# Optimization experiments

Hardware: AMD Instinct MI355X
Metric: run time of the kernel (lower is better)

Reference implementation:

```python
import jax, jax.numpy as jnp
import numpy as np

DIM, H, MAX_K, RADIUS, KNN_K, ALPHA, LN_EPS = 128, 4, 32, 0.3, 8, 2, 1e-5
DH = DIM // H
SCALE = DH ** -0.5


def _layernorm(x, w, b):
    mu = jnp.mean(x, axis=-1, keepdims=True)
    var = jnp.mean((x - mu) ** 2, axis=-1, keepdims=True)
    return (x - mu) * jax.lax.rsqrt(var + LN_EPS) * w + b


def setup_inputs() -> dict:
    key = jax.random.key(0)
    ks = jax.random.split(key, 12)
    N, M = 50000, 2500
    init = lambda k, shape: (jax.random.normal(k, shape, jnp.float32) * 0.02)
    return {
        "xyz": jax.random.normal(ks[0], (N, 3), jnp.float32),
        "feats": jax.random.normal(ks[1], (N, DIM), jnp.float32),
        "Wq": init(ks[2], (DIM, DIM)),
        "Wk": init(ks[3], (DIM, DIM)),
        "Wv": init(ks[4], (DIM, DIM)),
        "Wo": init(ks[5], (DIM, DIM)),
        "bo": jnp.zeros((DIM,), jnp.float32),
        "n1w": jnp.ones((DIM,), jnp.float32),
        "n1b": jnp.zeros((DIM,), jnp.float32),
        "n2w": jnp.ones((DIM,), jnp.float32),
        "n2b": jnp.zeros((DIM,), jnp.float32),
        "W1": init(ks[6], (DIM, 4 * DIM)),
        "b1": jnp.zeros((4 * DIM,), jnp.float32),
        "W2": init(ks[7], (4 * DIM, DIM)),
        "b2": jnp.zeros((DIM,), jnp.float32),
        "Wp": init(ks[8], (DIM, DIM)),
        "bp": jnp.zeros((DIM,), jnp.float32),
        "idx_center": jax.random.randint(ks[9], (M,), 0, N),
    }


def reference(xyz, feats, Wq, Wk, Wv, Wo, bo, n1w, n1b, n2w, n2b, W1, b1, W2, b2, Wp, bp, idx_center):
    M = idx_center.shape[0]
    center_xyz = xyz[idx_center]          # (M,3)
    center_feat = feats[idx_center]       # (M,C)

    # euclidean distance matrix (M,N) via |a|^2+|b|^2-2ab, safe sqrt (0-grad at 0 like torch.cdist)
    d2 = (jnp.sum(center_xyz ** 2, -1)[:, None] + jnp.sum(xyz ** 2, -1)[None, :]
          - 2.0 * center_xyz @ xyz.T)
    d2 = jnp.maximum(d2, 0.0)
    pos = d2 > 0
    dist = jnp.where(pos, jnp.sqrt(jnp.where(pos, d2, 1.0)), 0.0)  # (M,N)

    # ball query: mask + top-max_k smallest distances
    nbr_mask = dist < RADIUS
    nbr_mask = nbr_mask.at[jnp.arange(M), idx_center].set(True)
    dist_masked = jnp.where(nbr_mask, dist, jnp.inf)
    neg_d, nbr_idx = jax.lax.top_k(-dist_masked, MAX_K)   # (M,K)
    nbr_dist = -neg_d
    mask_valid = jnp.isfinite(nbr_dist)                    # (M,K)

    # gather neighbor feats, zero where invalid
    nbr_feats = jnp.where(mask_valid[..., None], feats[nbr_idx], 0.0)  # (M,K,C)

    # masked local attention per center (tiny heads)
    q = (center_feat @ Wq).reshape(M, H, DH)                       # (M,H,D)
    k = (nbr_feats @ Wk).reshape(M, MAX_K, H, DH).transpose(0, 2, 1, 3)  # (M,H,K,D)
    v = (nbr_feats @ Wv).reshape(M, MAX_K, H, DH).transpose(0, 2, 1, 3)
    attn = jnp.einsum('mhd,mhkd->mhk', q * SCALE, k)
    attn = jnp.where(mask_valid[:, None, :], attn, -1e9)
    attn = jax.nn.softmax(attn, axis=-1)
    out = jnp.einsum('mhk,mhkd->mhd', attn, v)
    # faithful to torch: transpose(1,2) before flatten -> (M, D, H) layout
    out = jnp.swapaxes(out, 1, 2).reshape(M, DIM)
    upd = out @ Wo + bo

    cf = center_feat + _layernorm(upd, n1w, n1b)
    ffn = jax.nn.relu(cf @ W1 + b1) @ W2 + b2
    cf = cf + _layernorm(ffn, n2w, n2b)

    # KNN inverse-distance-weighted upsample back to all N points
    neg_v, knn_idx = jax.lax.top_k(-dist.T, KNN_K)   # (N,k)
    knn_dist = -neg_v
    w = 1.0 / (knn_dist + 1e-6) ** ALPHA
    w = w / jnp.sum(w, axis=-1, keepdims=True)
    out_feats = jnp.einsum('nk,nkc->nc', w, cf[knn_idx])  # (N,C)
    out_feats = out_feats + jax.nn.relu(out_feats @ Wp + bp)
    return feats + out_feats
```

## Files before the change

### kernel.cpp

```cpp
#include <hip/hip_runtime.h>
#include <hip/hip_bf16.h>
#include <stdint.h>

#define DIM    128
#define KMAX   32
#define LN_EPS 1e-5f
#define ATT_SCALE 0.17677669529663687f
#define CANDB  1024
#define WTOT   214400
#define PB     32
#define CH     64
#define GSTR   68

typedef unsigned long long u64;
static __device__ __forceinline__ float bf2f(__hip_bfloat16 x) { return __bfloat162float(x); }

static __device__ __forceinline__ float norm32(float x, float y, float z) {
    return __fadd_rn(__fadd_rn(__fmul_rn(x, x), __fmul_rn(y, y)), __fmul_rn(z, z));
}
static __device__ __forceinline__ float d2_32(float cx, float cy, float cz, float cw,
                                              float px, float py, float pz, float pw) {
    float dot = __fmaf_rn(cz, pz, __fmaf_rn(cy, py, __fmul_rn(cx, px)));
    return __fsub_rn(__fadd_rn(cw, pw), __fmul_rn(2.0f, dot));
}
static __device__ __forceinline__ float d2_to_dist(float d2) {
    d2 = fmaxf(d2, 0.0f);
    return (d2 > 0.0f) ? __fsqrt_rn(d2) : 0.0f;
}
static __device__ __forceinline__ float dist32(float cx, float cy, float cz, float cw,
                                               float px, float py, float pz, float pw) {
    return d2_to_dist(d2_32(cx, cy, cz, cw, px, py, pz, pw));
}

static __device__ __forceinline__ float ldf(const void* p, int f32, size_t i) {
    return f32 ? ((const float*)p)[i] : bf2f(((const __hip_bfloat16*)p)[i]);
}
static __device__ __forceinline__ int ldidx(const void* p, int i64, int m) {
    return i64 ? ((const int*)p)[2 * m] : ((const int*)p)[m];
}

struct Ptrs { const void* p[18]; int sz[18]; };

__global__ void probe_dtypes(Ptrs P, int* __restrict__ fl) {
    int j = threadIdx.x;
    if (j >= 18) return;
    const void* x = P.p[j];
    int sz = P.sz[j];
    int flag = 0;
    if (j == 17) {
        const int* ip = (const int*)x;
        int odd_zero = 1, even_nz = 0;
        for (int k = 0; k < 8 && 2 * k + 1 < sz * 2; ++k) {
            if (ip[2 * k + 1] != 0) odd_zero = 0;
            if (ip[2 * k] != 0) even_nz = 1;
        }
        flag = (odd_zero && even_nz) ? 1 : 0;
    } else {
        const __hip_bfloat16* hp = (const __hip_bfloat16*)x;
        int n = sz < 256 ? sz : 256;
        for (int i = 0; i < n; ++i) {
            float w = bf2f(hp[i]);
            if (w != w || fabsf(w) > 1000.0f) { flag = 1; break; }
        }
        if ((j == 7 || j == 9) && bf2f(hp[0]) == 0.0f) flag = 1;
    }
    fl[j] = flag;
}

__global__ __launch_bounds__(256) void conv_prep(Ptrs P, const int* __restrict__ fl,
                                                 float* __restrict__ Wf,
                                                 float4* __restrict__ pnt4,
                                                 float4* __restrict__ cent4,
                                                 int N, int M, int convB) {
    int b = blockIdx.x;
    if (b < convB) {
        int i = b * 256 + threadIdx.x;
        if (i >= WTOT) return;
        int j, off;
        if      (i < 16384)  { j = 2;  off = i; }
        else if (i < 32768)  { j = 3;  off = i - 16384; }
        else if (i < 49152)  { j = 4;  off = i - 32768; }
        else if (i < 65536)  { j = 5;  off = i - 49152; }
        else if (i < 131072) { j = 11; off = i - 65536; }
        else if (i < 196608) { j = 13; off = i - 131072; }
        else if (i < 212992) { j = 15; off = i - 196608; }
        else if (i < 213120) { j = 6;  off = i - 212992; }
        else if (i < 213248) { j = 7;  off = i - 213120; }
        else if (i < 213376) { j = 8;  off = i - 213248; }
        else if (i < 213504) { j = 9;  off = i - 213376; }
        else if (i < 213632) { j = 10; off = i - 213504; }
        else if (i < 214144) { j = 12; off = i - 213632; }
        else if (i < 214272) { j = 14; off = i - 214144; }
        else                 { j = 16; off = i - 214272; }
        Wf[i] = ldf(P.p[j], fl[j], off);
    } else {
        int i = (b - convB) * 256 + threadIdx.x;
        int f0 = fl[0];
        if (i < N) {
            float x = ldf(P.p[0], f0, 3 * i + 0);
            float y = ldf(P.p[0], f0, 3 * i + 1);
            float z = ldf(P.p[0], f0, 3 * i + 2);
            pnt4[i] = make_float4(x, y, z, norm32(x, y, z));
        }
        if (i < M) {
            int c = ldidx(P.p[17], fl[17], i);
            c = (c >= 0 && c < N) ? c : 0;
            float x = ldf(P.p[0], f0, 3 * c + 0);
            float y = ldf(P.p[0], f0, 3 * c + 1);
            float z = ldf(P.p[0], f0, 3 * c + 2);
            cent4[i] = make_float4(x, y, z, norm32(x, y, z));
        }
    }
}

__global__ __launch_bounds__(256, 8) void ball_scan(
    const float4* __restrict__ pnt4,
    const float4* __restrict__ cent4,
    int N, int M, int* __restrict__ nbr_g) {

    __shared__ u64 key[2][CANDB];
    __shared__ int s_cnt[2], s_ni[2][KMAX];

    int tid = threadIdx.x;
    int m0 = blockIdx.x * 2, m1 = m0 + 1;
    bool has1 = (m1 < M);
    float4 c0 = cent4[m0];
    float4 c1 = has1 ? cent4[m1] : make_float4(1e30f, 1e30f, 1e30f, 1e30f);

    if (tid < 2) s_cnt[tid] = 0;
    if (tid < KMAX) { s_ni[0][tid] = -1; s_ni[1][tid] = -1; }
    __syncthreads();

    for (int i = tid; i < N; i += 512) {
        int i2 = i + 256;
        float4 p = pnt4[i];
        float4 q = (i2 < N) ? pnt4[i2] : make_float4(1e30f, 1e30f, 1e30f, 1e30f);

        float dA0 = d2_32(c0.x, c0.y, c0.z, c0.w, p.x, p.y, p.z, p.w);
        float dA1 = d2_32(c1.x, c1.y, c1.z, c1.w, p.x, p.y, p.z, p.w);
        float dB0 = d2_32(c0.x, c0.y, c0.z, c0.w, q.x, q.y, q.z, q.w);
        float dB1 = d2_32(c1.x, c1.y, c1.z, c1.w, q.x, q.y, q.z, q.w);

        if (dA0 < 0.0901f) {
            float dist = d2_to_dist(dA0);
            if (dist < 0.3f) {
                int pos = atomicAdd(&s_cnt[0], 1);
                if (pos < CANDB)
                    key[0][pos] = ((u64)__float_as_uint(dist) << 32) | (unsigned)i;
            }
        }
        if (dA1 < 0.0901f) {
            float dist = d2_to_dist(dA1);
            if (dist < 0.3f) {
                int pos = atomicAdd(&s_cnt[1], 1);
                if (pos < CANDB)
                    key[1][pos] = ((u64)__float_as_uint(dist) << 32) | (unsigned)i;
            }
        }
        if (i2 < N) {
            if (dB0 < 0.0901f) {
                float dist = d2_to_dist(dB0);
                if (dist < 0.3f) {
                    int pos = atomicAdd(&s_cnt[0], 1);
                    if (pos < CANDB)
                        key[0][pos] = ((u64)__float_as_uint(dist) << 32) | (unsigned)i2;
                }
            }
            if (dB1 < 0.0901f) {
                float dist = d2_to_dist(dB1);
                if (dist < 0.3f) {
                    int pos = atomicAdd(&s_cnt[1], 1);
                    if (pos < CANDB)
                        key[1][pos] = ((u64)__float_as_uint(dist) << 32) | (unsigned)i2;
                }
            }
        }
    }
    __syncthreads();

    int half = tid >> 7, t2 = tid & 127;
    int cnth = min(s_cnt[half], CANDB);
    if (half == 1 && !has1) cnth = 0;
    for (int i = t2; i < cnth; i += 128) {
        u64 ki = key[half][i];
        int r = 0;
        for (int j = 0; j < cnth; ++j) r += (key[half][j] < ki) ? 1 : 0;
        if (r < KMAX) s_ni[half][r] = (int)(unsigned)(ki & 0xFFFFFFFFULL);
    }
    __syncthreads();
    if (tid < KMAX) nbr_g[m0 * KMAX + tid] = s_ni[0][tid];
    if (has1 && tid >= 128 && tid < 128 + KMAX)
        nbr_g[m1 * KMAX + (tid - 128)] = s_ni[1][tid - 128];
}

__global__ __launch_bounds__(512, 6) void attn_core(
    const int* __restrict__ nbr_g,
    const void* __restrict__ feats,
    const void* __restrict__ idxc,
    const int* __restrict__ fl,
    const float* __restrict__ Wf,
    float* __restrict__ cf_out, int N, int M) {

    const float* Wqf = Wf;
    const float* Wkf = Wf + 16384;
    const float* Wvf = Wf + 32768;
    const float* Wof = Wf + 49152;
    const float* Pf  = Wf + 212992;

    __shared__ __align__(16) float G[CH * GSTR];
    __shared__ __align__(16) float s_pv[16][128];
    __shared__ int   s_ni[2 * KMAX];
    __shared__ __align__(16) float s_cf[256], s_q[256], s_attn[256], s_ao[256];
    __shared__ float s_red[8];

    int tid = threadIdx.x;
    int lane = tid & 63, wv = tid >> 6;
    int m0 = blockIdx.x * 2;
    int f1 = fl[1], fi = fl[17];

    if (tid < 64) {
        int m2 = m0 + (tid >> 5);
        s_ni[tid] = (m2 < M) ? nbr_g[m2 * KMAX + (tid & 31)] : -1;
    }
    if (tid < 256) {
        int center = tid >> 7, col = tid & 127;
        int m2 = m0 + center; m2 = (m2 < M) ? m2 : (M - 1);
        int c = ldidx(idxc, fi, m2);
        c = (c >= 0 && c < N) ? c : 0;
        s_cf[tid] = ldf(feats, f1, (size_t)c * DIM + col);
    }
    __syncthreads();

    if (tid < 256) {
        int center = tid >> 7, col = tid & 127;
        float acc = 0.0f;
        const float* cfc = s_cf + center * 128;
#pragma unroll 4
        for (int i = 0; i < DIM; i += 4) {
            float4 a = *(const float4*)&cfc[i];
            acc = fmaf(a.x, Wqf[(i + 0) * DIM + col], acc);
            acc = fmaf(a.y, Wqf[(i + 1) * DIM + col], acc);
            acc = fmaf(a.z, Wqf[(i + 2) * DIM + col], acc);
            acc = fmaf(a.w, Wqf[(i + 3) * DIM + col], acc);
        }
        s_q[tid] = acc;
    }

    int kq = tid >> 5;
    int cq = tid & 31;
    int k0 = kq * 4, c0 = cq * 4;
    int cent = kq >> 3;
    float ka[4][4], va[4][4];
#pragma unroll
    for (int j = 0; j < 4; ++j)
#pragma unroll
        for (int t = 0; t < 4; ++t) { ka[j][t] = 0.0f; va[j][t] = 0.0f; }

    for (int r = 0; r < 2; ++r) {
        if (r) __syncthreads();
        for (int t = tid; t < 64 * CH; t += 512) {
            int kk = t >> 6, cc = t & 63;
            int idx = s_ni[kk];
            float v = (idx >= 0 && idx < N)
                    ? ldf(feats, f1, (size_t)idx * DIM + r * CH + cc) : 0.0f;
            G[cc * GSTR + kk] = v;
        }
        __syncthreads();
#pragma unroll 2
        for (int i = 0; i < CH; ++i) {
            float4 n = *(const float4*)&G[i * GSTR + k0];
            int gi = r * CH + i;
            float4 wk  = *(const float4*)&Wkf[gi * DIM + c0];
            float4 wv4 = *(const float4*)&Wvf[gi * DIM + c0];
            float nn[4] = {n.x, n.y, n.z, n.w};
#pragma unroll
            for (int j = 0; j < 4; ++j) {
                float nj = nn[j];
                ka[j][0] = fmaf(nj, wk.x, ka[j][0]);
                ka[j][1] = fmaf(nj, wk.y, ka[j][1]);
                ka[j][2] = fmaf(nj, wk.z, ka[j][2]);
                ka[j][3] = fmaf(nj, wk.w, ka[j][3]);
                va[j][0] = fmaf(nj, wv4.x, va[j][0]);
                va[j][1] = fmaf(nj, wv4.y, va[j][1]);
                va[j][2] = fmaf(nj, wv4.z, va[j][2]);
                va[j][3] = fmaf(nj, wv4.w, va[j][3]);
            }
        }
    }

    {
        const float* qc = s_q + cent * 128;
        float part[4];
#pragma unroll
        for (int j = 0; j < 4; ++j) {
            float p = 0.0f;
            p = fmaf(qc[c0 + 0], ka[j][0], p);
            p = fmaf(qc[c0 + 1], ka[j][1], p);
            p = fmaf(qc[c0 + 2], ka[j][2], p);
            p = fmaf(qc[c0 + 3], ka[j][3], p);
            p += __shfl_xor(p, 1, 64);
            p += __shfl_xor(p, 2, 64);
            p += __shfl_xor(p, 4, 64);
            part[j] = p;
        }
        if ((cq & 7) == 0) {
            int h = cq >> 3;
#pragma unroll
            for (int j = 0; j < 4; ++j)
                s_attn[cent * 128 + h * 32 + (kq & 7) * 4 + j] = part[j];
        }
    }
    __syncthreads();

    if (tid < 256) {
        int center = tid >> 7;
        int kk = tid & 31;
        float s = s_attn[tid] * ATT_SCALE;
        if (s_ni[center * 32 + kk] < 0) s = -1e9f;
        float mx = s;
        for (int off = 16; off; off >>= 1) mx = fmaxf(mx, __shfl_xor(mx, off, 32));
        float e = expf(s - mx);
        float sm = e;
        for (int off = 16; off; off >>= 1) sm += __shfl_xor(sm, off, 32);
        sm = (sm > 0.0f) ? sm : 1.0f;
        s_attn[tid] = e / sm;
    }
    __syncthreads();

    {
        int h = cq >> 3;
        float pvp0 = 0.0f, pvp1 = 0.0f, pvp2 = 0.0f, pvp3 = 0.0f;
#pragma unroll
        for (int j = 0; j < 4; ++j) {
            float a = s_attn[cent * 128 + h * 32 + (kq & 7) * 4 + j];
            pvp0 = fmaf(a, va[j][0], pvp0);
            pvp1 = fmaf(a, va[j][1], pvp1);
            pvp2 = fmaf(a, va[j][2], pvp2);
            pvp3 = fmaf(a, va[j][3], pvp3);
        }
        *(float4*)&s_pv[kq][c0] = make_float4(pvp0, pvp1, pvp2, pvp3);
    }
    __syncthreads();

    if (tid < 256) {
        int cb = tid >> 7, cc2 = tid & 127;
        float o = s_pv[cb * 8 + 0][cc2];
        o += s_pv[cb * 8 + 1][cc2];
        o += s_pv[cb * 8 + 2][cc2];
        o += s_pv[cb * 8 + 3][cc2];
        o += s_pv[cb * 8 + 4][cc2];
        o += s_pv[cb * 8 + 5][cc2];
        o += s_pv[cb * 8 + 6][cc2];
        o += s_pv[cb * 8 + 7][cc2];
        s_ao[cb * 128 + (cc2 & 31) * 4 + (cc2 >> 5)] = o;
    }
    __syncthreads();

    float upd = 0.0f, xc = 0.0f;
    int center = tid >> 7, col = tid & 127;
    if (tid < 256) {
        upd = Pf[0 + col];
#pragma unroll 4
        for (int i = 0; i < DIM; i += 4) {
            float4 a = *(const float4*)&s_ao[center * 128 + i];
            upd = fmaf(a.x, Wof[(i + 0) * DIM + col], upd);
            upd = fmaf(a.y, Wof[(i + 1) * DIM + col], upd);
            upd = fmaf(a.z, Wof[(i + 2) * DIM + col], upd);
            upd = fmaf(a.w, Wof[(i + 3) * DIM + col], upd);
        }
        float sum = upd;
        for (int off = 32; off; off >>= 1) sum += __shfl_xor(sum, off, 64);
        if (lane == 0) s_red[wv] = sum;
    }
    __syncthreads();
    if (tid < 256) {
        float mu = (s_red[center * 2] + s_red[center * 2 + 1]) * (1.0f / 128.0f);
        xc = upd - mu;
        float q2 = xc * xc;
        for (int off = 32; off; off >>= 1) q2 += __shfl_xor(q2, off, 64);
        if (lane == 0) s_red[4 + wv] = q2;
    }
    __syncthreads();
    if (tid < 256) {
        float var = (s_red[4 + center * 2] + s_red[5 + center * 2]) * (1.0f / 128.0f);
        float rs = 1.0f / sqrtf(var + LN_EPS);
        float ln1 = fmaf(xc * rs, Pf[128 + col], Pf[256 + col]);
        float cf1 = s_cf[tid] + ln1;
        int m2 = m0 + center;
        if (m2 < M) cf_out[(size_t)m2 * DIM + col] = cf1;
    }
}

__global__ __launch_bounds__(256) void ffn_ln(
    const float* __restrict__ Wf,
    float* __restrict__ cf, int M) {

    const float* W1f = Wf + 65536;
    const float* W2f = Wf + 131072;
    const float* Pf  = Wf + 212992;

    __shared__ __align__(16) float s_x[512];
    __shared__ __align__(16) float s_h[2048];
    __shared__ float s_p2[2][4][128];
    __shared__ float s_red[8];

    int tid = threadIdx.x, lane = tid & 63, wv = tid >> 6;
    int m0 = blockIdx.x * 4;

    for (int t = tid; t < 512; t += 256) {
        int cent = t >> 7, c = t & 127;
        int m = m0 + cent;
        s_x[t] = (m < M) ? cf[(size_t)m * DIM + c] : 0.0f;
    }
    __syncthreads();

    {
        int pairh = tid >> 7;
        int j0 = (tid & 127) * 4;
        float4 b1q = *(const float4*)&Pf[640 + j0];
        float aA0 = b1q.x, aA1 = b1q.y, aA2 = b1q.z, aA3 = b1q.w;
        float aB0 = b1q.x, aB1 = b1q.y, aB2 = b1q.z, aB3 = b1q.w;
        const float* xA = s_x + (2 * pairh) * 128;
        const float* xB = s_x + (2 * pairh + 1) * 128;
#pragma unroll 2
        for (int i4 = 0; i4 < 32; ++i4) {
            float4 xa = *(const float4*)&xA[i4 * 4];
            float4 xb = *(const float4*)&xB[i4 * 4];
#pragma unroll
            for (int s = 0; s < 4; ++s) {
                float4 w = *(const float4*)&W1f[(i4 * 4 + s) * 512 + j0];
                float va_ = (&xa.x)[s], vb_ = (&xb.x)[s];
                aA0 = fmaf(va_, w.x, aA0); aA1 = fmaf(va_, w.y, aA1);
                aA2 = fmaf(va_, w.z, aA2); aA3 = fmaf(va_, w.w, aA3);
                aB0 = fmaf(vb_, w.x, aB0); aB1 = fmaf(vb_, w.y, aB1);
                aB2 = fmaf(vb_, w.z, aB2); aB3 = fmaf(vb_, w.w, aB3);
            }
        }
        *(float4*)&s_h[(2 * pairh) * 512 + j0] =
            make_float4(fmaxf(aA0, 0.0f), fmaxf(aA1, 0.0f), fmaxf(aA2, 0.0f), fmaxf(aA3, 0.0f));
        *(float4*)&s_h[(2 * pairh + 1) * 512 + j0] =
            make_float4(fmaxf(aB0, 0.0f), fmaxf(aB1, 0.0f), fmaxf(aB2, 0.0f), fmaxf(aB3, 0.0f));
    }
    __syncthreads();

    {
        int kh = tid >> 7;
        int c = tid & 127;
        float acc0 = (kh == 0) ? Pf[1152 + c] : 0.0f;
        float acc1 = acc0, acc2 = acc0, acc3 = acc0;
        const float* h0 = s_h + 0 * 512 + kh * 256;
        const float* h1 = s_h + 1 * 512 + kh * 256;
        const float* h2 = s_h + 2 * 512 + kh * 256;
        const float* h3 = s_h + 3 * 512 + kh * 256;
#pragma unroll 2
        for (int i4 = 0; i4 < 64; ++i4) {
            float4 q0 = *(const float4*)&h0[i4 * 4];
            float4 q1 = *(const float4*)&h1[i4 * 4];
            float4 q2 = *(const float4*)&h2[i4 * 4];
            float4 q3 = *(const float4*)&h3[i4 * 4];
#pragma unroll
            for (int s = 0; s < 4; ++s) {
                float w = W2f[(kh * 256 + i4 * 4 + s) * DIM + c];
                acc0 = fmaf((&q0.x)[s], w, acc0);
                acc1 = fmaf((&q1.x)[s], w, acc1);
                acc2 = fmaf((&q2.x)[s], w, acc2);
                acc3 = fmaf((&q3.x)[s], w, acc3);
            }
        }
        s_p2[kh][0][c] = acc0;
        s_p2[kh][1][c] = acc1;
        s_p2[kh][2][c] = acc2;
        s_p2[kh][3][c] = acc3;
    }
    __syncthreads();

    for (int rr = 0; rr < 2; ++rr) {
        int cl = tid >> 7;
        int cent = rr * 2 + cl;
        int c = tid & 127;
        float ffn = s_p2[0][cent][c] + s_p2[1][cent][c];
        float sum = ffn;
        for (int off = 32; off; off >>= 1) sum += __shfl_xor(sum, off, 64);
        if (lane == 0) s_red[wv] = sum;
        __syncthreads();
        float mu = (s_red[cl * 2] + s_red[cl * 2 + 1]) * (1.0f / 128.0f);
        float xc = ffn - mu;
        float q2 = xc * xc;
        for (int off = 32; off; off >>= 1) q2 += __shfl_xor(q2, off, 64);
        if (lane == 0) s_red[4 + wv] = q2;
        __syncthreads();
        float var = (s_red[4 + cl * 2] + s_red[5 + cl * 2]) * (1.0f / 128.0f);
        float rs2 = 1.0f / sqrtf(var + LN_EPS);
        float ln2 = fmaf(xc * rs2, Pf[384 + c], Pf[512 + c]);
        int m = m0 + cent;
        if (m < M) cf[(size_t)m * DIM + c] = s_x[cent * 128 + c] + ln2;
        __syncthreads();
    }
}

#define CSWAP(a, b) { if ((b) < (a)) { u64 t_ = (a); (a) = (b); (b) = t_; } }

static __device__ __forceinline__ float bound8(float vmn) {
    float v = vmn;
    v = fminf(v, __shfl_xor(v, 1, 64));
    v = fminf(v, __shfl_xor(v, 2, 64));
    v = fminf(v, __shfl_xor(v, 4, 64));
    v = fmaxf(v, __shfl_xor(v, 8, 64));
    v = fmaxf(v, __shfl_xor(v, 16, 64));
    v = fmaxf(v, __shfl_xor(v, 32, 64));
    return fmaxf(v, 0.0f) * 1.0000019073486328f;
}

__global__ __launch_bounds__(256) void knn_select(
    const float4* __restrict__ pnt4,
    const float4* __restrict__ cent4,
    const float* __restrict__ cf,
    float* __restrict__ upg,
    int N, int M) {

    __shared__ u64 s_buf[4][4][64];
    __shared__ u64 s_srt[4][4][8];
    __shared__ int s_cnt[4][4];

    int tid = threadIdx.x;
    int lane = tid & 63, wv = tid >> 6;
    int p0 = blockIdx.x * 16 + wv * 4;

    float4 pp[4];
    bool own[4];
#pragma unroll
    for (int e = 0; e < 4; ++e) {
        int p = p0 + e;
        own[e] = (p < N);
        pp[e] = own[e] ? pnt4[p] : make_float4(0.f, 0.f, 0.f, 0.f);
    }

    if (lane < 4) s_cnt[wv][lane] = 0;
    __syncthreads();

    float vmn[4] = {3.4e38f, 3.4e38f, 3.4e38f, 3.4e38f};
    for (int j = lane; j < M; j += 64) {
        float4 cc = cent4[j];
#pragma unroll
        for (int e = 0; e < 4; ++e)
            vmn[e] = fminf(vmn[e], d2_32(cc.x, cc.y, cc.z, cc.w,
                                         pp[e].x, pp[e].y, pp[e].z, pp[e].w));
    }
    float T[4];
#pragma unroll
    for (int e = 0; e < 4; ++e) T[e] = bound8(vmn[e]);

    for (int j = lane; j < M; j += 64) {
        float4 cc = cent4[j];
#pragma unroll
        for (int e = 0; e < 4; ++e) {
            float d2 = d2_32(cc.x, cc.y, cc.z, cc.w,
                             pp[e].x, pp[e].y, pp[e].z, pp[e].w);
            if (d2 <= T[e]) {
                float dist = d2_to_dist(d2);
                u64 key = ((u64)__float_as_uint(dist) << 32) | (unsigned)j;
                int pos = atomicAdd(&s_cnt[wv][e], 1);
                if (pos < 64) s_buf[wv][e][pos] = key;
            }
        }
    }

    int c0 = lane, c1 = lane + 64;
#pragma unroll
    for (int e = 0; e < 4; ++e) {
        int cnt = s_cnt[wv][e];
        if (cnt <= 64 && M >= 8) {
            u64 myk = (lane < cnt) ? s_buf[wv][e][lane] : ~0ULL;
            int r = 0;
            for (int i = 0; i < cnt; ++i) {
                u64 o = s_buf[wv][e][i];
                r += (o < myk) ? 1 : 0;
            }
            if (lane < cnt && r < 8) s_srt[wv][e][r] = myk;
        } else {
            float4 pq = pp[e];
            u64 f0 = ~0ULL, f1_ = ~0ULL, f2_ = ~0ULL, f3 = ~0ULL,
                f4 = ~0ULL, f5 = ~0ULL, f6 = ~0ULL, f7 = ~0ULL;
            for (int j = lane; j < M; j += 64) {
                float4 cc = cent4[j];
                float dist = dist32(cc.x, cc.y, cc.z, cc.w, pq.x, pq.y, pq.z, pq.w);
                u64 key = ((u64)__float_as_uint(dist) << 32) | (unsigned)j;
                if (key < f7) {
                    f7 = key;
                    CSWAP(f6, f7); CSWAP(f5, f6); CSWAP(f4, f5); CSWAP(f3, f4);
                    CSWAP(f2_, f3); CSWAP(f1_, f2_); CSWAP(f0, f1_);
                }
            }
            int ptr2 = 0;
            u64 cur2 = f0;
#pragma unroll
            for (int e2 = 0; e2 < 8; ++e2) {
                u64 v = cur2;
                for (int off = 32; off; off >>= 1) {
                    u64 o = __shfl_down(v, off, 64);
                    v = (o < v) ? o : v;
                }
                u64 gm = __shfl(v, 0, 64);
                if (lane == 0) s_srt[wv][e][e2] = gm;
                if (cur2 == gm) {
                    ptr2++;
                    cur2 = (ptr2 == 1) ? f1_ : (ptr2 == 2) ? f2_ : (ptr2 == 3) ? f3 :
                           (ptr2 == 4) ? f4 : (ptr2 == 5) ? f5 : (ptr2 == 6) ? f6 :
                           (ptr2 == 7) ? f7 : ~0ULL;
                }
            }
        }
        int   ki[8];
        float w8[8];
        float ws = 0.0f;
#pragma unroll
        for (int e2 = 0; e2 < 8; ++e2) {
            u64 gm = s_srt[wv][e][e2];
            float d = __uint_as_float((unsigned)(gm >> 32));
            int ci = (int)(unsigned)(gm & 0xFFFFFFFFULL);
            ci = (ci >= 0 && ci < M) ? ci : 0;
            float t = __fadd_rn(d, 1e-6f);
            float w = 1.0f / __fmul_rn(t, t);
            ws += w;
            ki[e2] = ci;
            w8[e2] = w;
        }
        float inv = 1.0f / ws;
#pragma unroll
        for (int k = 0; k < 8; ++k) w8[k] *= inv;

        float u0 = 0.0f, u1 = 0.0f;
#pragma unroll
        for (int k = 0; k < 8; ++k) {
            const float* row = cf + (size_t)ki[k] * DIM;
            u0 = fmaf(w8[k], row[c0], u0);
            u1 = fmaf(w8[k], row[c1], u1);
        }
        if (own[e]) {
            upg[(size_t)(p0 + e) * DIM + c0] = u0;
            upg[(size_t)(p0 + e) * DIM + c1] = u1;
        }
    }
}

__global__ __launch_bounds__(256) void wp_out(
    const float* __restrict__ Wf,
    const void* __restrict__ feats,
    const int* __restrict__ fl,
    float* __restrict__ out,
    int N) {

    const float* Wpf = Wf + 196608;
    const float* bpf = Wf + 212992 + 1280;

    __shared__ __align__(16) float s_up[PB][132];

    int tid = threadIdx.x;
    int p0 = blockIdx.x * PB;

    for (int f = tid; f < PB * 32; f += 256) {
        int p = f >> 5, i4 = (f & 31) << 2;
        float4 v = make_float4(0.f, 0.f, 0.f, 0.f);
        if (p0 + p < N) v = *(const float4*)&out[(size_t)(p0 + p) * DIM + i4];
        *(float4*)&s_up[p][i4] = v;
    }
    __syncthreads();

    int cq = tid & 31, pq = tid >> 5;
    int c0 = cq << 2;
    int pA = pq << 2;

    float a00 = 0.f, a01 = 0.f, a02 = 0.f, a03 = 0.f;
    float a10 = 0.f, a11 = 0.f, a12 = 0.f, a13 = 0.f;
    float a20 = 0.f, a21 = 0.f, a22 = 0.f, a23 = 0.f;
    float a30 = 0.f, a31 = 0.f, a32 = 0.f, a33 = 0.f;

#pragma unroll 4
    for (int i = 0; i < DIM; ++i) {
        float4 w = *(const float4*)&Wpf[(size_t)i * DIM + c0];
        float u0 = s_up[pA + 0][i];
        float u1 = s_up[pA + 1][i];
        float u2 = s_up[pA + 2][i];
        float u3 = s_up[pA + 3][i];
        a00 = fmaf(u0, w.x, a00); a01 = fmaf(u0, w.y, a01);
        a02 = fmaf(u0, w.z, a02); a03 = fmaf(u0, w.w, a03);
        a10 = fmaf(u1, w.x, a10); a11 = fmaf(u1, w.y, a11);
        a12 = fmaf(u1, w.z, a12); a13 = fmaf(u1, w.w, a13);
        a20 = fmaf(u2, w.x, a20); a21 = fmaf(u2, w.y, a21);
        a22 = fmaf(u2, w.z, a22); a23 = fmaf(u2, w.w, a23);
        a30 = fmaf(u3, w.x, a30); a31 = fmaf(u3, w.y, a31);
        a32 = fmaf(u3, w.z, a32); a33 = fmaf(u3, w.w, a33);
    }

    int f1v = fl[1];
    float4 bp4 = make_float4(bpf[c0 + 0], bpf[c0 + 1], bpf[c0 + 2], bpf[c0 + 3]);

    float accs[4][4] = {{a00, a01, a02, a03}, {a10, a11, a12, a13},
                        {a20, a21, a22, a23}, {a30, a31, a32, a33}};
#pragma unroll
    for (int a = 0; a < 4; ++a) {
        int p = p0 + pA + a;
        if (p < N) {
            float4 u = *(const float4*)&s_up[pA + a][c0];
            float4 o;
            o.x = ldf(feats, f1v, (size_t)p * DIM + c0 + 0) + u.x + fmaxf(bp4.x + accs[a][0], 0.0f);
            o.y = ldf(feats, f1v, (size_t)p * DIM + c0 + 1) + u.y + fmaxf(bp4.y + accs[a][1], 0.0f);
            o.z = ldf(feats, f1v, (size_t)p * DIM + c0 + 2) + u.z + fmaxf(bp4.z + accs[a][2], 0.0f);
            o.w = ldf(feats, f1v, (size_t)p * DIM + c0 + 3) + u.w + fmaxf(bp4.w + accs[a][3], 0.0f);
            *(float4*)&out[(size_t)p * DIM + c0] = o;
        }
    }
}

extern "C" void kernel_launch(void* const* d_in, const int* in_sizes, int n_in,
                              void* d_out, int out_size, void* d_ws, size_t ws_size,
                              hipStream_t stream) {
    int N = in_sizes[0] / 3;
    int M = in_sizes[17];

    Ptrs P;
    for (int j = 0; j < 18; ++j) { P.p[j] = d_in[j]; P.sz[j] = in_sizes[j]; }

    size_t off = 0;
    auto alloc = [&](size_t bytes) -> void* {
        off = (off + 255) & ~(size_t)255;
        void* p = (void*)((char*)d_ws + off);
        off += bytes;
        return p;
    };
    int*    fl    = (int*)alloc(32 * 4);
    float*  Wf    = (float*)alloc((size_t)WTOT * 4);
    float4* pnt4  = (float4*)alloc((size_t)N * 16);
    float4* cent4 = (float4*)alloc((size_t)M * 16);
    float*  cfbuf = (float*)alloc((size_t)M * DIM * 4);
    int*    nbr   = (int*)alloc((size_t)M * KMAX * 4);

    int convB = (WTOT + 255) / 256;
    int NM = (N > M) ? N : M;
    int prepB = (NM + 255) / 256;

    probe_dtypes<<<1, 32, 0, stream>>>(P, fl);
    conv_prep<<<convB + prepB, 256, 0, stream>>>(P, fl, Wf, pnt4, cent4, N, M, convB);
    ball_scan<<<(M + 1) / 2, 256, 0, stream>>>(pnt4, cent4, N, M, nbr);
    attn_core<<<(M + 1) / 2, 512, 0, stream>>>(nbr, d_in[1], d_in[17], fl, Wf, cfbuf, N, M);
    ffn_ln<<<(M + 3) / 4, 256, 0, stream>>>(Wf, cfbuf, M);
    knn_select<<<(N + 15) / 16, 256, 0, stream>>>(pnt4, cent4, cfbuf, (float*)d_out, N, M);
    wp_out<<<(N + PB - 1) / PB, 256, 0, stream>>>(Wf, d_in[1], fl, (float*)d_out, N);
}
```

Before: 466.3 us.

## Vectorize and prefetch neighbor feature gathers, split Q projection across all threads

The neighbor-feature gather into shared memory now uses 4-wide vector loads per thread, issued into registers early. The first chunk's load overlaps the Q projection and the second chunk's load overlaps the first chunk's K/V accumulation. The Q projection is split across all 512 threads as two half-dot-products, then reduced through shared scratch, so threads that used to sit idle now help. This costs more registers and one extra barrier, and adds a dependency on s_pv being free as scratch at this point.

```diff
diff --git a/kernel.cpp b/kernel.cpp
--- a/kernel.cpp
+++ b/kernel.cpp
@@ -37,6 +37,25 @@
 }
 static __device__ __forceinline__ int ldidx(const void* p, int i64, int m) {
     return i64 ? ((const int*)p)[2 * m] : ((const int*)p)[m];
+}
+
+static __device__ __forceinline__ void gload4(float* d, const void* p, int f32,
+                                              int idx, int off, int N) {
+    if (idx >= 0 && idx < N) {
+        if (f32) {
+            float4 v = *(const float4*)((const float*)p + (size_t)idx * DIM + off);
+            d[0] = v.x; d[1] = v.y; d[2] = v.z; d[3] = v.w;
+        } else {
+            const __hip_bfloat16* hp = (const __hip_bfloat16*)p + (size_t)idx * DIM + off;
+            ushort4 v = *(const ushort4*)hp;
+            d[0] = bf2f(*(const __hip_bfloat16*)&v.x);
+            d[1] = bf2f(*(const __hip_bfloat16*)&v.y);
+            d[2] = bf2f(*(const __hip_bfloat16*)&v.z);
+            d[3] = bf2f(*(const __hip_bfloat16*)&v.w);
+        }
+    } else {
+        d[0] = d[1] = d[2] = d[3] = 0.0f;
+    }
 }
 
 struct Ptrs { const void* p[18]; int sz[18]; };
@@ -231,20 +250,50 @@
     }
     __syncthreads();
 
-    if (tid < 256) {
-        int center = tid >> 7, col = tid & 127;
+    int gkA = tid >> 4;
+    int gcA = (tid & 15) * 4;
+    int gkB = (tid + 512) >> 4;
+    int gcB = gcA;
+    int giA = s_ni[gkA], giB = s_ni[gkB];
+
+    float pA[4], pB[4];
+    gload4(pA, feats, f1, giA, 0 * CH + gcA, N);
+    gload4(pB, feats, f1, giB, 0 * CH + gcB, N);
+
+    float* s_qp = (float*)s_pv;
+    {
+        int qh = tid >> 8;
+        int qt = tid & 255;
+        int center = qt >> 7, col = qt & 127;
         float acc = 0.0f;
         const float* cfc = s_cf + center * 128;
+        int ib = qh * 64;
 #pragma unroll 4
-        for (int i = 0; i < DIM; i += 4) {
+        for (int i = ib; i < ib + 64; i += 4) {
             float4 a = *(const float4*)&cfc[i];
             acc = fmaf(a.x, Wqf[(i + 0) * DIM + col], acc);
             acc = fmaf(a.y, Wqf[(i + 1) * DIM + col], acc);
             acc = fmaf(a.z, Wqf[(i + 2) * DIM + col], acc);
             acc = fmaf(a.w, Wqf[(i + 3) * DIM + col], acc);
         }
-        s_q[tid] = acc;
-    }
+        s_qp[qh * 256 + qt] = acc;
+    }
+
+    G[(gcA + 0) * GSTR + gkA] = pA[0];
+    G[(gcA + 1) * GSTR + gkA] = pA[1];
+    G[(gcA + 2) * GSTR + gkA] = pA[2];
+    G[(gcA + 3) * GSTR + gkA] = pA[3];
+    G[(gcB + 0) * GSTR + gkB] = pB[0];
+    G[(gcB + 1) * GSTR + gkB] = pB[1];
+    G[(gcB + 2) * GSTR + gkB] = pB[2];
+    G[(gcB + 3) * GSTR + gkB] = pB[3];
+    __syncthreads();
+
+    float qA[4], qB[4];
+    gload4(qA, feats, f1, giA, 1 * CH + gcA, N);
+    gload4(qB, feats, f1, giB, 1 * CH + gcB, N);
+
+    if (tid < 256) s_q[tid] = s_qp[tid] + s_qp[256 + tid];
 
     int kq = tid >> 5;
     int cq = tid & 31;
@@ -256,35 +305,55 @@
 #pragma unroll
         for (int t = 0; t < 4; ++t) { ka[j][t] = 0.0f; va[j][t] = 0.0f; }
 
-    for (int r = 0; r < 2; ++r) {
-        if (r) __syncthreads();
-        for (int t = tid; t < 64 * CH; t += 512) {
-            int kk = t >> 6, cc = t & 63;
-            int idx = s_ni[kk];
-            float v = (idx >= 0 && idx < N)
-                    ? ldf(feats, f1, (size_t)idx * DIM + r * CH + cc) : 0.0f;
-            G[cc * GSTR + kk] = v;
-        }
-        __syncthreads();
 #pragma unroll 2
-        for (int i = 0; i < CH; ++i) {
-            float4 n = *(const float4*)&G[i * GSTR + k0];
-            int gi = r * CH + i;
-            float4 wk  = *(const float4*)&Wkf[gi * DIM + c0];
-            float4 wv4 = *(const float4*)&Wvf[gi * DIM + c0];
-            float nn[4] = {n.x, n.y, n.z, n.w};
-#pragma unroll
-            for (int j = 0; j < 4; ++j) {
-                float nj = nn[j];
-                ka[j][0] = fmaf(nj, wk.x, ka[j][0]);
-                ka[j][1] = fmaf(nj, wk.y, ka[j][1]);
-                ka[j][2] = fmaf(nj, wk.z, ka[j][2]);
-                ka[j][3] = fmaf(nj, wk.w, ka[j][3]);
-                va[j][0] = fmaf(nj, wv4.x, va[j][0]);
-                va[j][1] = fmaf(nj, wv4.y, va[j][1]);
-                va[j][2] = fmaf(nj, wv4.z, va[j][2]);
-                va[j][3] = fmaf(nj, wv4.w, va[j][3]);
-            }
+    for (int i = 0; i < CH; ++i) {
+        float4 n = *(const float4*)&G[i * GSTR + k0];
+        float4 wk  = *(const float4*)&Wkf[i * DIM + c0];
+        float4 wv4 = *(const float4*)&Wvf[i * DIM + c0];
+        float nn[4] = {n.x, n.y, n.z, n.w};
+#pragma unroll
+        for (int j = 0; j < 4; ++j) {
+            float nj = nn[j];
+            ka[j][0] = fmaf(nj, wk.x, ka[j][0]);
+            ka[j][1] = fmaf(nj, wk.y, ka[j][1]);
+            ka[j][2] = fmaf(nj, wk.z, ka[j][2]);
+            ka[j][3] = fmaf(nj, wk.w, ka[j][3]);
+            va[j][0] = fmaf(nj, wv4.x, va[j][0]);
+            va[j][1] = fmaf(nj, wv4.y, va[j][1]);
+            va[j][2] = fmaf(nj, wv4.z, va[j][2]);
+            va[j][3] = fmaf(nj, wv4.w, va[j][3]);
+        }
+    }
+    __syncthreads();
+
+    G[(gcA + 0) * GSTR + gkA] = qA[0];
+    G[(gcA + 1) * GSTR + gkA] = qA[1];
+    G[(gcA + 2) * GSTR + gkA] = qA[2];
+    G[(gcA + 3) * GSTR + gkA] = qA[3];
+    G[(gcB + 0) * GSTR + gkB] = qB[0];
+    G[(gcB + 1) * GSTR + gkB] = qB[1];
+    G[(gcB + 2) * GSTR + gkB] = qB[2];
+    G[(gcB + 3) * GSTR + gkB] = qB[3];
+    __syncthreads();
+
+#pragma unroll 2
+    for (int i = 0; i < CH; ++i) {
+        float4 n = *(const float4*)&G[i * GSTR + k0];
+        int gi = CH + i;
+        float4 wk  = *(const float4*)&Wkf[gi * DIM + c0];
+        float4 wv4 = *(const float4*)&Wvf[gi * DIM + c0];
+        float nn[4] = {n.x, n.y, n.z, n.w};
+#pragma unroll
+        for (int j = 0; j < 4; ++j) {
+            float nj = nn[j];
+            ka[j][0] = fmaf(nj, wk.x, ka[j][0]);
+            ka[j][1] = fmaf(nj, wk.y, ka[j][1]);
+            ka[j][2] = fmaf(nj, wk.z, ka[j][2]);
+            ka[j][3] = fmaf(nj, wk.w, ka[j][3]);
+            va[j][0] = fmaf(nj, wv4.x, va[j][0]);
+            va[j][1] = fmaf(nj, wv4.y, va[j][1]);
+            va[j][2] = fmaf(nj, wv4.z, va[j][2]);
+            va[j][3] = fmaf(nj, wv4.w, va[j][3]);
         }
     }
 
```

New measurement: 454.8 us. 2.5% less time.
